# Optimization experiments

Hardware: AMD Instinct MI355X
Metric: run time of the kernel (lower is better)

The kernel has to match this reference:

```python
import jax, jax.numpy as jnp
import numpy as np

EPS_CIOU = 1e-7   # keras backend epsilon used inside compute_ciou
EPS = 1e-9        # label-encoder epsilon
ALPHA = 0.5
BETA = 6.0
NUM_CLASSES = 80
TOPK = 10


def compute_ciou(b1, b2):
    """Complete IoU between xyxy boxes b1 (gt) and b2 (pred), broadcastable (...,4)."""
    x1a, y1a, x2a, y2a = b1[..., 0], b1[..., 1], b1[..., 2], b1[..., 3]
    x1b, y1b, x2b, y2b = b2[..., 0], b2[..., 1], b2[..., 2], b2[..., 3]
    w1 = x2a - x1a
    h1 = y2a - y1a + EPS_CIOU
    w2 = x2b - x1b
    h2 = y2b - y1b + EPS_CIOU
    iw = jnp.clip(jnp.minimum(x2a, x2b) - jnp.maximum(x1a, x1b), 0.0, None)
    ih = jnp.clip(jnp.minimum(y2a, y2b) - jnp.maximum(y1a, y1b), 0.0, None)
    inter = iw * ih
    union = w1 * h1 + w2 * h2 - inter
    iou = inter / (union + EPS_CIOU)
    cw = jnp.maximum(x2a, x2b) - jnp.minimum(x1a, x1b)
    ch = jnp.maximum(y2a, y2b) - jnp.minimum(y1a, y1b)
    c2 = cw * cw + ch * ch + EPS_CIOU
    rho2 = ((x1b + x2b - x1a - x2a) ** 2 + (y1b + y2b - y1a - y2a) ** 2) / 4.0
    v = (4.0 / np.pi ** 2) * (jnp.arctan(w2 / h2) - jnp.arctan(w1 / h1)) ** 2
    a = v / (v - iou + (1.0 + EPS_CIOU))
    return iou - (rho2 / c2 + v * a)


def _forward(pd_scores, pd_bboxes, anc_points, gt_labels, gt_bboxes, mask_gt):
    B, A, C = pd_scores.shape
    M = gt_bboxes.shape[1]
    f32 = pd_scores.dtype
    mask_gt_b = mask_gt.astype(bool)                      # (B, M, 1)

    # --- candidate anchors whose center falls inside each gt box ---
    lt = gt_bboxes[:, :, None, :2]                        # (B, M, 1, 2)
    rb = gt_bboxes[:, :, None, 2:]
    anc = anc_points[None, None, :, :]                    # (1, 1, A, 2)
    deltas = jnp.concatenate([anc - lt, rb - anc], -1)    # (B, M, A, 4)
    mask_in_gts = deltas.min(-1) > EPS                    # (B, M, A)
    valid = mask_in_gts & mask_gt_b                       # (B, M, A)

    # --- alignment metric: score^alpha * ciou^beta ---
    ind = gt_labels.astype(jnp.int32)                     # (B, M)
    scores_g = jnp.take_along_axis(pd_scores, jnp.maximum(ind, 0)[:, None, :], axis=-1)  # (B, A, M)
    scores_g = jnp.where(ind[:, None, :] >= 0, scores_g, 0.0)
    scores_g = jnp.transpose(scores_g, (0, 2, 1))         # (B, M, A)
    bbox_scores = jnp.where(valid, scores_g, 0.0)
    iou = compute_ciou(gt_bboxes[:, :, None, :], pd_bboxes[:, None, :, :])  # (B, M, A)
    iou = jnp.maximum(iou, 0.0)
    overlaps = jnp.where(valid, iou, 0.0)
    align_metric = bbox_scores ** ALPHA * overlaps ** BETA

    # --- top-k anchor candidates per gt box ---
    _, topk_idxs = jax.lax.top_k(align_metric, TOPK)      # (B, M, K)
    topk_mask = jnp.broadcast_to(mask_gt_b, (B, M, TOPK))
    topk_idxs = jnp.where(topk_mask, topk_idxs, 0)
    bi = jnp.arange(B)[:, None, None]
    mi = jnp.arange(M)[None, :, None]
    counts = jnp.zeros((B, M, A), f32).at[bi, mi, topk_idxs].add(1.0)
    mask_topk = jnp.where(counts > 1, 0.0, counts)        # duplicates (masked gts) -> 0
    mask_pos = mask_topk * mask_in_gts.astype(f32) * mask_gt.astype(f32)  # (B, M, A)

    # --- break ties: anchor matched to >1 gt keeps highest-IoU gt ---
    fg_mask = mask_pos.sum(axis=1)                        # (B, A)
    mask_multi = jnp.broadcast_to(fg_mask[:, None, :] > 1, (B, M, A))
    is_max = jax.nn.one_hot(jnp.argmax(overlaps, axis=1), M, dtype=f32)  # (B, A, M)
    is_max = jnp.transpose(is_max, (0, 2, 1))             # (B, M, A)
    mask_pos = jnp.where(mask_multi, is_max, mask_pos)
    fg_mask = mask_pos.sum(axis=1)
    target_gt_idx = jnp.argmax(mask_pos, axis=1)          # (B, A)

    # --- gather targets ---
    flat_idx = target_gt_idx + jnp.arange(B, dtype=target_gt_idx.dtype)[:, None] * M
    target_bboxes = gt_bboxes.reshape(-1, 4)[flat_idx]    # (B, A, 4)
    target_labels = jnp.maximum(gt_labels.reshape(-1)[flat_idx], 0.0)
    target_scores = jax.nn.one_hot(target_labels.astype(jnp.int32), C, dtype=f32)  # (B, A, C)
    target_scores = jnp.where((fg_mask > 0)[..., None], target_scores, 0.0)

    # --- normalize class targets by alignment ---
    align_metric = align_metric * mask_pos
    pos_align = align_metric.max(axis=-1, keepdims=True)              # (B, M, 1)
    pos_overlaps = (overlaps * mask_pos).max(axis=-1, keepdims=True)  # (B, M, 1)
    norm = (align_metric * pos_overlaps / (pos_align + EPS)).max(axis=-2)[..., None]  # (B, A, 1)
    target_scores = target_scores * norm

    return (jax.lax.stop_gradient(target_bboxes),
            jax.lax.stop_gradient(target_scores),
            jax.lax.stop_gradient(fg_mask > 0))


def setup_inputs() -> dict:
    key = jax.random.key(0)
    k = jax.random.split(key, 6)
    B, A, C, M = 32, 8400, 80, 64
    IMG = 640.0
    pd_scores = jax.random.uniform(k[0], (B, A, C), jnp.float32)
    pb = jax.random.uniform(k[1], (B, A, 4), jnp.float32) * IMG
    pd_bboxes = jnp.concatenate([jnp.minimum(pb[..., :2], pb[..., 2:]),
                                 jnp.maximum(pb[..., :2], pb[..., 2:])], -1)
    anc_points = jax.random.uniform(k[2], (A, 2), jnp.float32) * IMG
    ctr = jax.random.uniform(k[3], (B, M, 2), jnp.float32) * IMG
    wh = jax.random.uniform(k[4], (B, M, 2), jnp.float32) * 200.0 + 20.0
    gt_bboxes = jnp.concatenate([ctr - wh / 2, ctr + wh / 2], -1)
    gt_labels = jax.random.randint(k[5], (B, M), 0, C).astype(jnp.float32)
    mask_gt = jnp.ones((B, M, 1), jnp.bool_)
    return {"pd_scores": pd_scores, "pd_bboxes": pd_bboxes, "anc_points": anc_points,
            "gt_labels": gt_labels, "gt_bboxes": gt_bboxes, "mask_gt": mask_gt}


def reference(pd_scores, pd_bboxes, anc_points, gt_labels, gt_bboxes, mask_gt):
    return _forward(pd_scores, pd_bboxes, anc_points, gt_labels, gt_bboxes, mask_gt)
```

## Files before the change

kernel.cpp:

```cpp
#include <hip/hip_runtime.h>
#include <cstdint>
#include <cstddef>

#define EPSC 1e-7f
#define EPS9 1e-9f
#define K4PI2 0.40528473456935108577f
#define NTOPK 10
#define GX 16
#define GY 16
#define NCELL (GX * GY)
#define POOLCAP 2048

__device__ __forceinline__ bool mask_at(const unsigned char* mb, int i, int wide) {
    if (wide) return reinterpret_cast<const unsigned int*>(mb)[i] != 0u;
    return mb[i] != 0;
}

__device__ __forceinline__ unsigned long long shfl_xor_u64(unsigned long long v, int off) {
    int lo = __shfl_xor((int)(unsigned)(v & 0xFFFFFFFFull), off);
    int hi = __shfl_xor((int)(unsigned)(v >> 32), off);
    return ((unsigned long long)(unsigned)hi << 32) | (unsigned)lo;
}

__device__ __forceinline__ unsigned lane_rank(unsigned long long ball) {
    return __builtin_amdgcn_mbcnt_hi((unsigned)(ball >> 32),
           __builtin_amdgcn_mbcnt_lo((unsigned)(ball & 0xFFFFFFFFull), 0u));
}

__device__ __forceinline__ float ciou_clip(float x1a, float y1a, float x2a, float y2a,
                                           float w1h1, float atan1,
                                           float4 pb, float at2) {
    float w2 = pb.z - pb.x, h2 = pb.w - pb.y + EPSC;
    float iw = fmaxf(fminf(x2a, pb.z) - fmaxf(x1a, pb.x), 0.f);
    float ih = fmaxf(fminf(y2a, pb.w) - fmaxf(y1a, pb.y), 0.f);
    float inter = iw * ih;
    float uni = w1h1 + w2 * h2 - inter;
    float iou = inter / (uni + EPSC);
    float cw = fmaxf(x2a, pb.z) - fminf(x1a, pb.x);
    float ch = fmaxf(y2a, pb.w) - fminf(y1a, pb.y);
    float c2 = cw * cw + ch * ch + EPSC;
    float dx = pb.x + pb.z - x1a - x2a;
    float dy = pb.y + pb.w - y1a - y2a;
    float rho2 = (dx * dx + dy * dy) * 0.25f;
    float dat = at2 - atan1;
    float vv = K4PI2 * dat * dat;
    float aa = vv / (vv - iou + (1.f + EPSC));
    return fmaxf(iou - (rho2 / c2 + vv * aa), 0.f);
}

__global__ __launch_bounds__(1024) void k_prep(
    const unsigned char* __restrict__ mask, int nmask, int* __restrict__ mode,
    const float* __restrict__ anc, int A,
    int* __restrict__ cell_start, int* __restrict__ binned, float* __restrict__ gp)
{
    __shared__ int h[NCELL];
    __shared__ int cs[NCELL + 1];
    __shared__ int cur[NCELL];
    __shared__ float rmnx[16], rmny[16], rmxx[16], rmxy[16];
    __shared__ float s_gp[4];
    __shared__ int bad;

    int tid = threadIdx.x;
    int lane = tid & 63, wid = tid >> 6;
    const float2* an2 = reinterpret_cast<const float2*>(anc);

    if (tid == 0) bad = 0;
    if (tid < NCELL) h[tid] = 0;
    __syncthreads();

    const unsigned int* mw = reinterpret_cast<const unsigned int*>(mask);
    int nw = nmask >> 2;
    for (int i = tid; i < nw; i += 1024) {
        unsigned int v = mw[i];
        if (v != 0u && v != 1u && v != 0x3f800000u) atomicOr(&bad, 1);
    }

    float mnx = 3e38f, mny = 3e38f, mxx = -3e38f, mxy = -3e38f;
    for (int i = tid; i < A; i += 1024) {
        float2 p = an2[i];
        mnx = fminf(mnx, p.x); mny = fminf(mny, p.y);
        mxx = fmaxf(mxx, p.x); mxy = fmaxf(mxy, p.y);
    }
#pragma unroll
    for (int off = 32; off; off >>= 1) {
        mnx = fminf(mnx, __shfl_xor(mnx, off));
        mny = fminf(mny, __shfl_xor(mny, off));
        mxx = fmaxf(mxx, __shfl_xor(mxx, off));
        mxy = fmaxf(mxy, __shfl_xor(mxy, off));
    }
    if (lane == 0) { rmnx[wid] = mnx; rmny[wid] = mny; rmxx[wid] = mxx; rmxy[wid] = mxy; }
    __syncthreads();
    if (tid == 0) {
        mode[0] = bad ? 0 : 1;
        float a = 3e38f, b2 = 3e38f, c = -3e38f, d = -3e38f;
        for (int i = 0; i < 16; ++i) {
            a = fminf(a, rmnx[i]); b2 = fminf(b2, rmny[i]);
            c = fmaxf(c, rmxx[i]); d = fmaxf(d, rmxy[i]);
        }
        float rx = fmaxf(c - a, 1e-6f), ry = fmaxf(d - b2, 1e-6f);
        s_gp[0] = a; s_gp[1] = b2;
        s_gp[2] = (float)GX / rx; s_gp[3] = (float)GY / ry;
        gp[0] = s_gp[0]; gp[1] = s_gp[1]; gp[2] = s_gp[2]; gp[3] = s_gp[3];
    }
    __syncthreads();
    float ox = s_gp[0], oy = s_gp[1], ivx = s_gp[2], ivy = s_gp[3];

    for (int i = tid; i < A; i += 1024) {
        float2 p = an2[i];
        int cx = min(GX - 1, max(0, (int)floorf((p.x - ox) * ivx)));
        int cy = min(GY - 1, max(0, (int)floorf((p.y - oy) * ivy)));
        atomicAdd(&h[cy * GX + cx], 1);
    }
    __syncthreads();
    if (wid == 0) {
        int base = 0;
        for (int ch = 0; ch < NCELL / 64; ++ch) {
            int v = h[ch * 64 + lane];
            int inc = v;
            for (int off = 1; off < 64; off <<= 1) {
                int u = __shfl_up(inc, off);
                if (lane >= off) inc += u;
            }
            cs[ch * 64 + lane] = base + inc - v;
            base += __shfl(inc, 63);
        }
        if (lane == 0) cs[NCELL] = base;
    }
    __syncthreads();
    if (tid <= NCELL) cell_start[tid] = cs[tid];
    if (tid < NCELL) cur[tid] = cs[tid];
    __syncthreads();
    for (int i = tid; i < A; i += 1024) {
        float2 p = an2[i];
        int cx = min(GX - 1, max(0, (int)floorf((p.x - ox) * ivx)));
        int cy = min(GY - 1, max(0, (int)floorf((p.y - oy) * ivy)));
        int slot = atomicAdd(&cur[cy * GX + cx], 1);
        binned[slot] = i;
    }
}

#define INTEST(ap) ((ap.x - x1a > EPS9) & (ap.y - y1a > EPS9) & \
                    (x2a - ap.x > EPS9) & (y2a - ap.y > EPS9))

__global__ __launch_bounds__(256) void k_sel(
    const float* __restrict__ pd_scores, const float* __restrict__ pd_bboxes,
    const float* __restrict__ anc, const float* __restrict__ gt_labels,
    const float* __restrict__ gt_bboxes, const unsigned char* __restrict__ mask_gt,
    const int* __restrict__ mode, const int* __restrict__ cell_start,
    const int* __restrict__ binned, const float* __restrict__ gp,
    int* __restrict__ count, int* __restrict__ win_idx, float* __restrict__ win_al,
    int* __restrict__ win_fl, int* __restrict__ ovf,
    int A, int C, int M, int B)
{
    __shared__ unsigned long long pool[POOLCAP];
    __shared__ int sP[GY + 1];
    __shared__ int sB[GY];
    __shared__ int s_n, s_ovf;

    int bid = blockIdx.x;
    int b = bid % B, m = bid / B;
    int row = b * M + m;
    if (!mask_at(mask_gt, row, mode[0])) return;
    int tid = threadIdx.x;
    int lane = tid & 63, wid = tid >> 6;

    float4 g = reinterpret_cast<const float4*>(gt_bboxes)[row];
    float x1a = g.x, y1a = g.y, x2a = g.z, y2a = g.w;
    float w1 = x2a - x1a, h1 = y2a - y1a + EPSC;
    float w1h1 = w1 * h1;
    float atan1 = atanf(w1 / h1);
    int lbl = (int)gt_labels[row];

    float ox = gp[0], oy = gp[1], ivx = gp[2], ivy = gp[3];
    int cx0 = min(GX - 1, max(0, (int)floorf((x1a - ox) * ivx)));
    int cx1 = min(GX - 1, max(0, (int)floorf((x2a - ox) * ivx)));
    int cy0 = min(GY - 1, max(0, (int)floorf((y1a - oy) * ivy)));
    int cy1 = min(GY - 1, max(0, (int)floorf((y2a - oy) * ivy)));
    int ns = cy1 - cy0 + 1;

    if (tid == 0) {
        s_n = 0; s_ovf = 0;
        int P = 0;
        for (int s2 = 0; s2 < ns; ++s2) {
            int cbase = (cy0 + s2) * GX;
            int S = cell_start[cbase + cx0];
            int E = cell_start[cbase + cx1 + 1];
            sP[s2] = P; sB[s2] = S - P; P += E - S;
        }
        sP[ns] = P;
    }
    __syncthreads();
    int L = sP[ns];

    const float2* an2 = reinterpret_cast<const float2*>(anc);
    const float4* pb4 = reinterpret_cast<const float4*>(pd_bboxes + (size_t)b * A * 4);
    const float*  ps  = pd_scores + (size_t)b * A * C;

    int sptr = 0;
    for (int f0 = tid; f0 < L; f0 += 1024) {
        int f1 = f0 + 256, f2 = f0 + 512, f3 = f0 + 768;
        bool o1 = f1 < L, o2 = f2 < L, o3 = f3 < L;
        while (f0 >= sP[sptr + 1]) ++sptr;
        int sl0 = sB[sptr] + f0;
        int sp = sptr;
        if (o1) { while (f1 >= sP[sp + 1]) ++sp; }
        int sl1 = sB[sp] + f1;
        if (o2) { while (f2 >= sP[sp + 1]) ++sp; }
        int sl2 = sB[sp] + f2;
        if (o3) { while (f3 >= sP[sp + 1]) ++sp; }
        int sl3 = sB[sp] + f3;

        int a0 = binned[sl0];
        int a1 = o1 ? binned[sl1] : 0;
        int a2 = o2 ? binned[sl2] : 0;
        int a3 = o3 ? binned[sl3] : 0;
        float2 ap0 = an2[a0], ap1 = an2[a1], ap2 = an2[a2], ap3 = an2[a3];
        bool in0 = INTEST(ap0);
        bool in1 = o1 & INTEST(ap1);
        bool in2 = o2 & INTEST(ap2);
        bool in3 = o3 & INTEST(ap3);

        float4 pb0, pb1, pb2, pb3;
        float sc0 = 0.f, sc1 = 0.f, sc2 = 0.f, sc3 = 0.f;
        if (in0) { pb0 = pb4[a0]; if (lbl >= 0) sc0 = ps[(size_t)a0 * C + lbl]; }
        if (in1) { pb1 = pb4[a1]; if (lbl >= 0) sc1 = ps[(size_t)a1 * C + lbl]; }
        if (in2) { pb2 = pb4[a2]; if (lbl >= 0) sc2 = ps[(size_t)a2 * C + lbl]; }
        if (in3) { pb3 = pb4[a3]; if (lbl >= 0) sc3 = ps[(size_t)a3 * C + lbl]; }

#define PROC(ink, ak, pbk, sck) { \
        unsigned long long key = 0; \
        if (ink) { \
            float w2 = pbk.z - pbk.x, h2 = pbk.w - pbk.y + EPSC; \
            float at2 = atanf(w2 / h2); \
            float ovl = ciou_clip(x1a, y1a, x2a, y2a, w1h1, atan1, pbk, at2); \
            float o2v = ovl * ovl; \
            float val = sqrtf(sck) * (o2v * o2v * o2v); \
            key = ((unsigned long long)__float_as_uint(val) << 32) | (unsigned)(~(unsigned)ak); \
        } \
        unsigned long long ball = __ballot(ink); \
        if (ball) { \
            int bs = 0; \
            if (lane == 0) bs = atomicAdd(&s_n, __popcll(ball)); \
            bs = __shfl(bs, 0); \
            if (ink) { \
                int pos = bs + (int)lane_rank(ball); \
                if (pos < POOLCAP) pool[pos] = key; else s_ovf = 1; \
            } \
        } }
        PROC(in0, a0, pb0, sc0)
        PROC(in1, a1, pb1, sc1)
        PROC(in2, a2, pb2, sc2)
        PROC(in3, a3, pb3, sc3)
#undef PROC
    }
    __syncthreads();
    if (s_ovf || s_n > POOLCAP) {
        if (tid == 0) ovf[row] = 1;
        return;
    }
    if (wid != 0) return;

    int n = s_n;
    unsigned long long tv[NTOPK];
#pragma unroll
    for (int j = 0; j < NTOPK; ++j) tv[j] = 0;
    int pcnt = 0;
    for (int i = lane; i < n; i += 64) {
        unsigned long long kk = pool[i];
        pcnt += (kk >> 32) ? 1 : 0;
        if (kk > tv[NTOPK - 1]) {
            tv[NTOPK - 1] = kk;
#pragma unroll
            for (int j = NTOPK - 1; j > 0; --j)
                if (tv[j] > tv[j - 1]) { unsigned long long t = tv[j]; tv[j] = tv[j - 1]; tv[j - 1] = t; }
        }
    }
#pragma unroll
    for (int off = 32; off; off >>= 1) pcnt += __shfl_xor(pcnt, off);
    int p = pcnt;
    int rp = p < NTOPK ? p : NTOPK;
    size_t bA = (size_t)b * A;
    int base_o = row * NTOPK;

    for (int k = 0; k < rp; ++k) {
        unsigned long long head = tv[0];
        unsigned long long best = head;
#pragma unroll
        for (int off = 32; off; off >>= 1) {
            unsigned long long o = shfl_xor_u64(best, off);
            if (o > best) best = o;
        }
        if (head == best && head != 0ull) {
            int a = (int)(~(unsigned)(best & 0xFFFFFFFFull));
            int o = base_o + k;
            win_idx[o] = a;
            win_al[o]  = __uint_as_float((unsigned)(best >> 32));
            win_fl[o]  = 1;
            atomicAdd(&count[bA + a], 1);
#pragma unroll
            for (int j = 0; j < NTOPK - 1; ++j) tv[j] = tv[j + 1];
            tv[NTOPK - 1] = 0;
        }
    }

    if (rp < NTOPK) {
        int iters = (A + 63 - lane) / 64;
        int zp = 0;
        for (int k = rp; k < NTOPK; ++k) {
            unsigned zprop = 0xFFFFFFFFu;
            while (zp < iters) {
                int a = lane + zp * 64;
                float2 ap = an2[a];
                bool in = INTEST(ap);
                if (!in) { zprop = (unsigned)a; break; }
                ++zp;
            }
            unsigned cprop = 0xFFFFFFFFu;
#pragma unroll
            for (int j = 0; j < NTOPK; ++j) {
                unsigned long long kk = tv[j];
                if (kk != 0ull && kk < (1ull << 32)) {
                    unsigned idx2 = ~(unsigned)kk;
                    if (idx2 < cprop) cprop = idx2;
                }
            }
            unsigned prop = zprop < cprop ? zprop : cprop;
            unsigned bm_ = prop;
#pragma unroll
            for (int off = 32; off; off >>= 1) {
                unsigned o = (unsigned)__shfl_xor((int)bm_, off);
                if (o < bm_) bm_ = o;
            }
            if (bm_ != 0xFFFFFFFFu) {
                if (cprop == bm_ && cprop < zprop) {
                    int o = base_o + k;
                    win_idx[o] = (int)bm_; win_al[o] = 0.f; win_fl[o] = 1;
                    atomicAdd(&count[bA + bm_], 1);
                    unsigned long long wkk = (unsigned long long)(unsigned)(~bm_);
#pragma unroll
                    for (int j = 0; j < NTOPK; ++j) if (tv[j] == wkk) tv[j] = 0;
                } else if (zprop == bm_ && zprop < cprop) {
                    ++zp;
                }
            }
        }
    }
}

__global__ __launch_bounds__(64) void k_sel_fb(
    const float* __restrict__ pd_scores, const float* __restrict__ pd_bboxes,
    const float* __restrict__ anc, const float* __restrict__ gt_labels,
    const float* __restrict__ gt_bboxes, const unsigned char* __restrict__ mask_gt,
    const int* __restrict__ mode, const int* __restrict__ cell_start,
    const int* __restrict__ binned, const float* __restrict__ gp,
    const int* __restrict__ ovf,
    int* __restrict__ count, int* __restrict__ win_idx, float* __restrict__ win_al,
    int* __restrict__ win_fl,
    int A, int C, int M)
{
    int row = blockIdx.x;
    if (!ovf[row]) return;
    if (!mask_at(mask_gt, row, mode[0])) return;
    int b = row / M;
    int lane = threadIdx.x;

    float4 g = reinterpret_cast<const float4*>(gt_bboxes)[row];
    float x1a = g.x, y1a = g.y, x2a = g.z, y2a = g.w;
    float w1 = x2a - x1a, h1 = y2a - y1a + EPSC;
    float w1h1 = w1 * h1;
    float atan1 = atanf(w1 / h1);
    int lbl = (int)gt_labels[row];

    float ox = gp[0], oy = gp[1], ivx = gp[2], ivy = gp[3];
    int cx0 = min(GX - 1, max(0, (int)floorf((x1a - ox) * ivx)));
    int cx1 = min(GX - 1, max(0, (int)floorf((x2a - ox) * ivx)));
    int cy0 = min(GY - 1, max(0, (int)floorf((y1a - oy) * ivy)));
    int cy1 = min(GY - 1, max(0, (int)floorf((y2a - oy) * ivy)));

    const float2* an2 = reinterpret_cast<const float2*>(anc);
    const float4* pb4 = reinterpret_cast<const float4*>(pd_bboxes + (size_t)b * A * 4);
    const float*  ps  = pd_scores + (size_t)b * A * C;

    unsigned long long tv[NTOPK];
#pragma unroll
    for (int j = 0; j < NTOPK; ++j) tv[j] = 0;
    int pcnt = 0;

    for (int cy = cy0; cy <= cy1; ++cy) {
        int c0 = cy * GX + cx0;
        int s = cell_start[c0], e = cell_start[cy * GX + cx1 + 1];
        for (int i = s + lane; i < e; i += 64) {
            int a = binned[i];
            float2 ap = an2[a];
            bool in = INTEST(ap);
            if (in) {
                float4 pb = pb4[a];
                float w2 = pb.z - pb.x, h2 = pb.w - pb.y + EPSC;
                float at2 = atanf(w2 / h2);
                float ovl = ciou_clip(x1a, y1a, x2a, y2a, w1h1, atan1, pb, at2);
                float sc = (lbl >= 0) ? ps[(size_t)a * C + lbl] : 0.f;
                float o2 = ovl * ovl;
                float val = sqrtf(sc) * (o2 * o2 * o2);
                pcnt += (val > 0.f) ? 1 : 0;
                unsigned long long kk =
                    ((unsigned long long)__float_as_uint(val) << 32) | (unsigned)(~(unsigned)a);
                if (kk > tv[NTOPK - 1]) {
                    tv[NTOPK - 1] = kk;
#pragma unroll
                    for (int j = NTOPK - 1; j > 0; --j)
                        if (tv[j] > tv[j - 1]) {
                            unsigned long long t = tv[j]; tv[j] = tv[j - 1]; tv[j - 1] = t;
                        }
                }
            }
        }
    }

#pragma unroll
    for (int off = 32; off; off >>= 1) pcnt += __shfl_xor(pcnt, off);
    int p = pcnt;
    int rp = p < NTOPK ? p : NTOPK;
    size_t bA = (size_t)b * A;
    int base_o = row * NTOPK;

    for (int k = 0; k < rp; ++k) {
        unsigned long long head = tv[0];
        unsigned long long best = head;
#pragma unroll
        for (int off = 32; off; off >>= 1) {
            unsigned long long o = shfl_xor_u64(best, off);
            if (o > best) best = o;
        }
        if (head == best && head != 0ull) {
            int a = (int)(~(unsigned)(best & 0xFFFFFFFFull));
            int o = base_o + k;
            win_idx[o] = a;
            win_al[o]  = __uint_as_float((unsigned)(best >> 32));
            win_fl[o]  = 1;
            atomicAdd(&count[bA + a], 1);
#pragma unroll
            for (int j = 0; j < NTOPK - 1; ++j) tv[j] = tv[j + 1];
            tv[NTOPK - 1] = 0;
        }
    }

    if (rp < NTOPK) {
        int iters = (A + 63 - lane) / 64;
        int zp = 0;
        for (int k = rp; k < NTOPK; ++k) {
            unsigned zprop = 0xFFFFFFFFu;
            while (zp < iters) {
                int a = lane + zp * 64;
                float2 ap = an2[a];
                bool in = INTEST(ap);
                if (!in) { zprop = (unsigned)a; break; }
                ++zp;
            }
            unsigned cprop = 0xFFFFFFFFu;
#pragma unroll
            for (int j = 0; j < NTOPK; ++j) {
                unsigned long long kk = tv[j];
                if (kk != 0ull && kk < (1ull << 32)) {
                    unsigned idx2 = ~(unsigned)kk;
                    if (idx2 < cprop) cprop = idx2;
                }
            }
            unsigned prop = zprop < cprop ? zprop : cprop;
            unsigned bm_ = prop;
#pragma unroll
            for (int off = 32; off; off >>= 1) {
                unsigned o = (unsigned)__shfl_xor((int)bm_, off);
                if (o < bm_) bm_ = o;
            }
            if (bm_ != 0xFFFFFFFFu) {
                if (cprop == bm_ && cprop < zprop) {
                    int o = base_o + k;
                    win_idx[o] = (int)bm_; win_al[o] = 0.f; win_fl[o] = 1;
                    atomicAdd(&count[bA + bm_], 1);
                    unsigned long long wkk = (unsigned long long)(unsigned)(~bm_);
#pragma unroll
                    for (int j = 0; j < NTOPK; ++j) if (tv[j] == wkk) tv[j] = 0;
                } else if (zprop == bm_ && zprop < cprop) {
                    ++zp;
                }
            }
        }
    }
}

__global__ void k_resolve(
    const float* __restrict__ pd_scores, const float* __restrict__ pd_bboxes,
    const float* __restrict__ anc, const float* __restrict__ gt_labels,
    const float* __restrict__ gt_bboxes, const unsigned char* __restrict__ mask_gt,
    const int* __restrict__ mode,
    const int* __restrict__ count, const int* __restrict__ win_idx,
    const float* __restrict__ win_al, const int* __restrict__ win_fl,
    int* __restrict__ claim_m, float* __restrict__ claim_al,
    float* __restrict__ pos_al, float* __restrict__ pos_ov,
    int A, int C, int M, int total)
{
    int t = blockIdx.x * 256 + threadIdx.x;
    if (t >= total) return;
    int bm = t / NTOPK;
    int b = bm / M, m = bm % M;
    if (!win_fl[t]) return;
    int a = win_idx[t];
    size_t ba = (size_t)b * A + a;
    int cnt = count[ba];
    float al, ov; int mm_out;
    if (cnt == 1) {
        mm_out = m; al = win_al[t];
        float4 gg = reinterpret_cast<const float4*>(gt_bboxes)[b * M + m];
        float w1 = gg.z - gg.x, h1 = gg.w - gg.y + EPSC;
        float4 pb = reinterpret_cast<const float4*>(pd_bboxes)[ba];
        float w2 = pb.z - pb.x, h2p = pb.w - pb.y + EPSC;
        ov = ciou_clip(gg.x, gg.y, gg.z, gg.w, w1 * h1, atanf(w1 / h1), pb, atanf(w2 / h2p));
    } else {
        int wide = mode[0];
        float4 pb = reinterpret_cast<const float4*>(pd_bboxes)[ba];
        float2 ap = reinterpret_cast<const float2*>(anc)[a];
        float w2 = pb.z - pb.x, h2p = pb.w - pb.y + EPSC;
        float at2 = atanf(w2 / h2p);
        float best_ov = -1.f; int best_m = 0, best_valid = 0;
        for (int mm = 0; mm < M; ++mm) {
            float4 gg = reinterpret_cast<const float4*>(gt_bboxes)[b * M + mm];
            bool in = (ap.x - gg.x > EPS9) && (ap.y - gg.y > EPS9) &&
                      (gg.z - ap.x > EPS9) && (gg.w - ap.y > EPS9);
            bool valid = in && mask_at(mask_gt, b * M + mm, wide);
            float ovv = 0.f;
            if (valid) {
                float w1 = gg.z - gg.x, h1 = gg.w - gg.y + EPSC;
                ovv = ciou_clip(gg.x, gg.y, gg.z, gg.w, w1 * h1, atanf(w1 / h1), pb, at2);
            }
            if (ovv > best_ov) { best_ov = ovv; best_m = mm; best_valid = valid ? 1 : 0; }
        }
        int lb = (int)gt_labels[b * M + best_m];
        float sc = (best_valid && lb >= 0) ? pd_scores[ba * C + lb] : 0.f;
        float o2 = best_ov * best_ov;
        mm_out = best_m; al = sqrtf(sc) * (o2 * o2 * o2); ov = best_ov;
    }
    claim_m[ba]  = mm_out;
    claim_al[ba] = al;
    atomicMax((unsigned int*)&pos_al[b * M + mm_out], __float_as_uint(al));
    atomicMax((unsigned int*)&pos_ov[b * M + mm_out], __float_as_uint(ov));
}

__global__ __launch_bounds__(256) void k_final(
    const int* __restrict__ count, const int* __restrict__ claim_m,
    const float* __restrict__ claim_al,
    const float* __restrict__ pos_al, const float* __restrict__ pos_ov,
    const float* __restrict__ gt_labels, const float* __restrict__ gt_bboxes,
    float* __restrict__ out_bb, float* __restrict__ out_ts, float* __restrict__ out_fg,
    int A, int M, int C4, int BA)
{
    __shared__ float s_nv[256];
    __shared__ int   s_lb[256];
    int base_ba = blockIdx.x * 256;
    int tid = threadIdx.x;
    int ba = base_ba + tid;
    if (ba < BA) {
        int b = ba / A;
        int cnt = count[ba];
        int m = claim_m[ba];
        float4 g = reinterpret_cast<const float4*>(gt_bboxes)[b * M + m];
        reinterpret_cast<float4*>(out_bb)[ba] = g;
        float nv = 0.f; int lb = -1;
        if (cnt > 0) {
            lb = max((int)gt_labels[b * M + m], 0);
            nv = claim_al[ba] * pos_ov[b * M + m] / (pos_al[b * M + m] + EPS9);
        }
        out_fg[ba] = (cnt > 0) ? 1.f : 0.f;
        s_nv[tid] = nv; s_lb[tid] = lb;
    } else { s_nv[tid] = 0.f; s_lb[tid] = -1; }
    __syncthreads();
    float4* ts4 = reinterpret_cast<float4*>(out_ts);
    size_t fbase = (size_t)base_ba * C4;
    for (int j = 0; j < C4; ++j) {
        int fl = j * 256 + tid;
        int la = fl / C4;
        int ch = fl - la * C4;
        int ba2 = base_ba + la;
        if (ba2 < BA) {
            float nv = s_nv[la];
            int lb = s_lb[la];
            int c0 = ch * 4;
            float4 o;
            o.x = (c0     == lb) ? nv : 0.f;
            o.y = (c0 + 1 == lb) ? nv : 0.f;
            o.z = (c0 + 2 == lb) ? nv : 0.f;
            o.w = (c0 + 3 == lb) ? nv : 0.f;
            ts4[fbase + fl] = o;
        }
    }
}

extern "C" void kernel_launch(void* const* d_in, const int* in_sizes, int n_in,
                              void* d_out, int out_size, void* d_ws, size_t ws_size,
                              hipStream_t stream) {
    const float* pd_scores = (const float*)d_in[0];
    const float* pd_bboxes = (const float*)d_in[1];
    const float* anc       = (const float*)d_in[2];
    const float* gt_labels = (const float*)d_in[3];
    const float* gt_bboxes = (const float*)d_in[4];
    const unsigned char* mask_gt = (const unsigned char*)d_in[5];

    int A  = in_sizes[2] / 2;
    int BA = in_sizes[1] / 4;
    int B  = BA / A;
    int C  = in_sizes[0] / BA;
    int M  = in_sizes[3] / B;
    int BM = B * M;

    char* w = (char*)d_ws;
    auto alloc = [&](size_t bytes) { char* p = w; w += ((bytes + 255) / 256) * 256; return p; };
    int*   mode       = (int*)  alloc(256);
    char*  zero_beg   = w;
    int*   count      = (int*)  alloc((size_t)BA * 4);
    int*   claim_m    = (int*)  alloc((size_t)BA * 4);
    float* pos_al     = (float*)alloc((size_t)BM * 4);
    float* pos_ov     = (float*)alloc((size_t)BM * 4);
    int*   win_fl     = (int*)  alloc((size_t)BM * NTOPK * 4);
    int*   ovf        = (int*)  alloc((size_t)BM * 4);
    char*  zero_end   = w;
    float* claim_al   = (float*)alloc((size_t)BA * 4);
    int*   win_idx    = (int*)  alloc((size_t)BM * NTOPK * 4);
    float* win_al     = (float*)alloc((size_t)BM * NTOPK * 4);
    int*   cell_start = (int*)  alloc((size_t)(NCELL + 1) * 4);
    int*   binned     = (int*)  alloc((size_t)A * 4);
    float* gp         = (float*)alloc(256);

    float* out_bb = (float*)d_out;
    float* out_ts = out_bb + (size_t)BA * 4;
    float* out_fg = out_ts + (size_t)BA * C;

    hipMemsetAsync(zero_beg, 0, (size_t)(zero_end - zero_beg), stream);

    k_prep<<<1, 1024, 0, stream>>>(mask_gt, BM, mode, anc, A, cell_start, binned, gp);
    k_sel<<<BM, 256, 0, stream>>>(pd_scores, pd_bboxes, anc, gt_labels, gt_bboxes, mask_gt,
                                  mode, cell_start, binned, gp,
                                  count, win_idx, win_al, win_fl, ovf, A, C, M, B);
    k_sel_fb<<<BM, 64, 0, stream>>>(pd_scores, pd_bboxes, anc, gt_labels, gt_bboxes, mask_gt,
                                    mode, cell_start, binned, gp, ovf,
                                    count, win_idx, win_al, win_fl, A, C, M);
    int nclaims = BM * NTOPK;
    k_resolve<<<(nclaims + 255) / 256, 256, 0, stream>>>(
        pd_scores, pd_bboxes, anc, gt_labels, gt_bboxes, mask_gt, mode,
        count, win_idx, win_al, win_fl, claim_m, claim_al, pos_al, pos_ov, A, C, M, nclaims);
    int C4 = C / 4;
    int gBA = (BA + 255) / 256;
    k_final<<<gBA, 256, 0, stream>>>(count, claim_m, claim_al, pos_al, pos_ov,
                                     gt_labels, gt_bboxes, out_bb, out_ts, out_fg, A, M, C4, BA);
}
```

Baseline: 97.08 us.

## Fold fallback into selection kernel, zero outputs separately, sparse target-score writes

The separate overflow fallback kernel is removed; overflowing rows now run the warp-level scan inline inside k_sel, which eliminates one launch and the ovf buffer. The workspace memset becomes a custom zeroing kernel, and a second zeroing kernel clears the whole dense target-score output. The final kernel then writes only the single nonzero class per positive anchor instead of composing every float4 of the dense output. claim_m is moved out of the zeroed range and is read only when the count is positive. Box loads in k_sel are made unconditional so they can be issued early, at the cost of extra loads for anchors that fail the in-box test.

```diff
diff --git a/kernel.cpp b/kernel.cpp
--- a/kernel.cpp
+++ b/kernel.cpp
@@ -48,6 +48,11 @@
     return fmaxf(iou - (rho2 / c2 + vv * aa), 0.f);
 }
 
+__global__ void k_zero(float4* __restrict__ p, int n4) {
+    int i = blockIdx.x * 256 + threadIdx.x;
+    if (i < n4) p[i] = make_float4(0.f, 0.f, 0.f, 0.f);
+}
+
 __global__ __launch_bounds__(1024) void k_prep(
     const unsigned char* __restrict__ mask, int nmask, int* __restrict__ mode,
     const float* __restrict__ anc, int A,
@@ -142,6 +147,111 @@
 #define INTEST(ap) ((ap.x - x1a > EPS9) & (ap.y - y1a > EPS9) & \
                     (x2a - ap.x > EPS9) & (y2a - ap.y > EPS9))
 
+__device__ void fb_scan(
+    int lane, int A, int C, float x1a, float y1a, float x2a, float y2a,
+    float w1h1, float atan1, int lbl,
+    int cx0, int cx1, int cy0, int cy1,
+    const float2* an2, const float4* pb4, const float* ps,
+    const int* cell_start, const int* binned,
+    int* count, int* win_idx, float* win_al, int* win_fl,
+    size_t bA, int base_o)
+{
+    unsigned long long tv[NTOPK];
+#pragma unroll
+    for (int j = 0; j < NTOPK; ++j) tv[j] = 0;
+    int pcnt = 0;
+    for (int cy = cy0; cy <= cy1; ++cy) {
+        int s = cell_start[cy * GX + cx0], e = cell_start[cy * GX + cx1 + 1];
+        for (int i = s + lane; i < e; i += 64) {
+            int a = binned[i];
+            float2 ap = an2[a];
+            bool in = INTEST(ap);
+            if (in) {
+                float4 pb = pb4[a];
+                float w2 = pb.z - pb.x, h2 = pb.w - pb.y + EPSC;
+                float at2 = atanf(w2 / h2);
+                float ovl = ciou_clip(x1a, y1a, x2a, y2a, w1h1, atan1, pb, at2);
+                float sc = (lbl >= 0) ? ps[(size_t)a * C + lbl] : 0.f;
+                float o2 = ovl * ovl;
+                float val = sqrtf(sc) * (o2 * o2 * o2);
+                pcnt += (val > 0.f) ? 1 : 0;
+                unsigned long long kk =
+                    ((unsigned long long)__float_as_uint(val) << 32) | (unsigned)(~(unsigned)a);
+                if (kk > tv[NTOPK - 1]) {
+                    tv[NTOPK - 1] = kk;
+#pragma unroll
+                    for (int j = NTOPK - 1; j > 0; --j)
+                        if (tv[j] > tv[j - 1]) {
+                            unsigned long long t = tv[j]; tv[j] = tv[j - 1]; tv[j - 1] = t;
+                        }
+                }
+            }
+        }
+    }
+#pragma unroll
+    for (int off = 32; off; off >>= 1) pcnt += __shfl_xor(pcnt, off);
+    int rp = pcnt < NTOPK ? pcnt : NTOPK;
+    for (int k = 0; k < rp; ++k) {
+        unsigned long long head = tv[0];
+        unsigned long long best = head;
+#pragma unroll
+        for (int off = 32; off; off >>= 1) {
+            unsigned long long o = shfl_xor_u64(best, off);
+            if (o > best) best = o;
+        }
+        if (head == best && head != 0ull) {
+            int a = (int)(~(unsigned)(best & 0xFFFFFFFFull));
+            int o = base_o + k;
+            win_idx[o] = a; win_al[o] = __uint_as_float((unsigned)(best >> 32)); win_fl[o] = 1;
+            atomicAdd(&count[bA + a], 1);
+#pragma unroll
+            for (int j = 0; j < NTOPK - 1; ++j) tv[j] = tv[j + 1];
+            tv[NTOPK - 1] = 0;
+        }
+    }
+    if (rp < NTOPK) {
+        int iters = (A + 63 - lane) / 64;
+        int zp = 0;
+        for (int k = rp; k < NTOPK; ++k) {
+            unsigned zprop = 0xFFFFFFFFu;
+            while (zp < iters) {
+                int a = lane + zp * 64;
+                float2 ap = an2[a];
+                if (!INTEST(ap)) { zprop = (unsigned)a; break; }
+                ++zp;
+            }
+            unsigned cprop = 0xFFFFFFFFu;
+#pragma unroll
+            for (int j = 0; j < NTOPK; ++j) {
+                unsigned long long kk = tv[j];
+                if (kk != 0ull && kk < (1ull << 32)) {
+                    unsigned idx2 = ~(unsigned)kk;
+                    if (idx2 < cprop) cprop = idx2;
+                }
+            }
+            unsigned prop = zprop < cprop ? zprop : cprop;
+            unsigned bm_ = prop;
+#pragma unroll
+            for (int off = 32; off; off >>= 1) {
+                unsigned o = (unsigned)__shfl_xor((int)bm_, off);
+                if (o < bm_) bm_ = o;
+            }
+            if (bm_ != 0xFFFFFFFFu) {
+                if (cprop == bm_ && cprop < zprop) {
+                    int o = base_o + k;
+                    win_idx[o] = (int)bm_; win_al[o] = 0.f; win_fl[o] = 1;
+                    atomicAdd(&count[bA + bm_], 1);
+                    unsigned long long wkk = (unsigned long long)(unsigned)(~bm_);
+#pragma unroll
+                    for (int j = 0; j < NTOPK; ++j) if (tv[j] == wkk) tv[j] = 0;
+                } else if (zprop == bm_ && zprop < cprop) {
+                    ++zp;
+                }
+            }
+        }
+    }
+}
+
 __global__ __launch_bounds__(256) void k_sel(
     const float* __restrict__ pd_scores, const float* __restrict__ pd_bboxes,
     const float* __restrict__ anc, const float* __restrict__ gt_labels,
@@ -149,7 +259,7 @@
     const int* __restrict__ mode, const int* __restrict__ cell_start,
     const int* __restrict__ binned, const float* __restrict__ gp,
     int* __restrict__ count, int* __restrict__ win_idx, float* __restrict__ win_al,
-    int* __restrict__ win_fl, int* __restrict__ ovf,
+    int* __restrict__ win_fl,
     int A, int C, int M, int B)
 {
     __shared__ unsigned long long pool[POOLCAP];
@@ -157,8 +267,8 @@
     __shared__ int sB[GY];
     __shared__ int s_n, s_ovf;
 
-    int bid = blockIdx.x;
-    int b = bid % B, m = bid / B;
+    int rid = blockIdx.x;
+    int b = rid % B, m = rid / B;
     int row = b * M + m;
     if (!mask_at(mask_gt, row, mode[0])) return;
     int tid = threadIdx.x;
@@ -195,6 +305,8 @@
     const float2* an2 = reinterpret_cast<const float2*>(anc);
     const float4* pb4 = reinterpret_cast<const float4*>(pd_bboxes + (size_t)b * A * 4);
     const float*  ps  = pd_scores + (size_t)b * A * C;
+    size_t bA = (size_t)b * A;
+    int base_o = row * NTOPK;
 
     int sptr = 0;
     for (int f0 = tid; f0 < L; f0 += 1024) {
@@ -215,17 +327,17 @@
         int a2 = o2 ? binned[sl2] : 0;
         int a3 = o3 ? binned[sl3] : 0;
         float2 ap0 = an2[a0], ap1 = an2[a1], ap2 = an2[a2], ap3 = an2[a3];
+        float4 pb0 = pb4[a0], pb1 = pb4[a1], pb2 = pb4[a2], pb3 = pb4[a3];
         bool in0 = INTEST(ap0);
         bool in1 = o1 & INTEST(ap1);
         bool in2 = o2 & INTEST(ap2);
         bool in3 = o3 & INTEST(ap3);
 
-        float4 pb0, pb1, pb2, pb3;
         float sc0 = 0.f, sc1 = 0.f, sc2 = 0.f, sc3 = 0.f;
-        if (in0) { pb0 = pb4[a0]; if (lbl >= 0) sc0 = ps[(size_t)a0 * C + lbl]; }
-        if (in1) { pb1 = pb4[a1]; if (lbl >= 0) sc1 = ps[(size_t)a1 * C + lbl]; }
-        if (in2) { pb2 = pb4[a2]; if (lbl >= 0) sc2 = ps[(size_t)a2 * C + lbl]; }
-        if (in3) { pb3 = pb4[a3]; if (lbl >= 0) sc3 = ps[(size_t)a3 * C + lbl]; }
+        if (in0 && lbl >= 0) sc0 = ps[(size_t)a0 * C + lbl];
+        if (in1 && lbl >= 0) sc1 = ps[(size_t)a1 * C + lbl];
+        if (in2 && lbl >= 0) sc2 = ps[(size_t)a2 * C + lbl];
+        if (in3 && lbl >= 0) sc3 = ps[(size_t)a3 * C + lbl];
 
 #define PROC(ink, ak, pbk, sck) { \
         unsigned long long key = 0; \
@@ -255,7 +367,10 @@
     }
     __syncthreads();
     if (s_ovf || s_n > POOLCAP) {
-        if (tid == 0) ovf[row] = 1;
+        if (wid == 0)
+            fb_scan(lane, A, C, x1a, y1a, x2a, y2a, w1h1, atan1, lbl,
+                    cx0, cx1, cy0, cy1, an2, pb4, ps, cell_start, binned,
+                    count, win_idx, win_al, win_fl, bA, base_o);
         return;
     }
     if (wid != 0) return;
@@ -279,8 +394,6 @@
     for (int off = 32; off; off >>= 1) pcnt += __shfl_xor(pcnt, off);
     int p = pcnt;
     int rp = p < NTOPK ? p : NTOPK;
-    size_t bA = (size_t)b * A;
-    int base_o = row * NTOPK;
 
     for (int k = 0; k < rp; ++k) {
         unsigned long long head = tv[0];
@@ -311,149 +424,7 @@
             while (zp < iters) {
                 int a = lane + zp * 64;
                 float2 ap = an2[a];
-                bool in = INTEST(ap);
-                if (!in) { zprop = (unsigned)a; break; }
-                ++zp;
-            }
-            unsigned cprop = 0xFFFFFFFFu;
-#pragma unroll
-            for (int j = 0; j < NTOPK; ++j) {
-                unsigned long long kk = tv[j];
-                if (kk != 0ull && kk < (1ull << 32)) {
-                    unsigned idx2 = ~(unsigned)kk;
-                    if (idx2 < cprop) cprop = idx2;
-                }
-            }
-            unsigned prop = zprop < cprop ? zprop : cprop;
-            unsigned bm_ = prop;
-#pragma unroll
-            for (int off = 32; off; off >>= 1) {
-                unsigned o = (unsigned)__shfl_xor((int)bm_, off);
-                if (o < bm_) bm_ = o;
-            }
-            if (bm_ != 0xFFFFFFFFu) {
-                if (cprop == bm_ && cprop < zprop) {
-                    int o = base_o + k;
-                    win_idx[o] = (int)bm_; win_al[o] = 0.f; win_fl[o] = 1;
-                    atomicAdd(&count[bA + bm_], 1);
-                    unsigned long long wkk = (unsigned long long)(unsigned)(~bm_);
-#pragma unroll
-                    for (int j = 0; j < NTOPK; ++j) if (tv[j] == wkk) tv[j] = 0;
-                } else if (zprop == bm_ && zprop < cprop) {
-                    ++zp;
-                }
-            }
-        }
-    }
-}
-
-__global__ __launch_bounds__(64) void k_sel_fb(
-    const float* __restrict__ pd_scores, const float* __restrict__ pd_bboxes,
-    const float* __restrict__ anc, const float* __restrict__ gt_labels,
-    const float* __restrict__ gt_bboxes, const unsigned char* __restrict__ mask_gt,
-    const int* __restrict__ mode, const int* __restrict__ cell_start,
-    const int* __restrict__ binned, const float* __restrict__ gp,
-    const int* __restrict__ ovf,
-    int* __restrict__ count, int* __restrict__ win_idx, float* __restrict__ win_al,
-    int* __restrict__ win_fl,
-    int A, int C, int M)
-{
-    int row = blockIdx.x;
-    if (!ovf[row]) return;
-    if (!mask_at(mask_gt, row, mode[0])) return;
-    int b = row / M;
-    int lane = threadIdx.x;
-
-    float4 g = reinterpret_cast<const float4*>(gt_bboxes)[row];
-    float x1a = g.x, y1a = g.y, x2a = g.z, y2a = g.w;
-    float w1 = x2a - x1a, h1 = y2a - y1a + EPSC;
-    float w1h1 = w1 * h1;
-    float atan1 = atanf(w1 / h1);
-    int lbl = (int)gt_labels[row];
-
-    float ox = gp[0], oy = gp[1], ivx = gp[2], ivy = gp[3];
-    int cx0 = min(GX - 1, max(0, (int)floorf((x1a - ox) * ivx)));
-    int cx1 = min(GX - 1, max(0, (int)floorf((x2a - ox) * ivx)));
-    int cy0 = min(GY - 1, max(0, (int)floorf((y1a - oy) * ivy)));
-    int cy1 = min(GY - 1, max(0, (int)floorf((y2a - oy) * ivy)));
-
-    const float2* an2 = reinterpret_cast<const float2*>(anc);
-    const float4* pb4 = reinterpret_cast<const float4*>(pd_bboxes + (size_t)b * A * 4);
-    const float*  ps  = pd_scores + (size_t)b * A * C;
-
-    unsigned long long tv[NTOPK];
-#pragma unroll
-    for (int j = 0; j < NTOPK; ++j) tv[j] = 0;
-    int pcnt = 0;
-
-    for (int cy = cy0; cy <= cy1; ++cy) {
-        int c0 = cy * GX + cx0;
-        int s = cell_start[c0], e = cell_start[cy * GX + cx1 + 1];
-        for (int i = s + lane; i < e; i += 64) {
-            int a = binned[i];
-            float2 ap = an2[a];
-            bool in = INTEST(ap);
-            if (in) {
-                float4 pb = pb4[a];
-                float w2 = pb.z - pb.x, h2 = pb.w - pb.y + EPSC;
-                float at2 = atanf(w2 / h2);
-                float ovl = ciou_clip(x1a, y1a, x2a, y2a, w1h1, atan1, pb, at2);
-                float sc = (lbl >= 0) ? ps[(size_t)a * C + lbl] : 0.f;
-                float o2 = ovl * ovl;
-                float val = sqrtf(sc) * (o2 * o2 * o2);
-                pcnt += (val > 0.f) ? 1 : 0;
-                unsigned long long kk =
-                    ((unsigned long long)__float_as_uint(val) << 32) | (unsigned)(~(unsigned)a);
-                if (kk > tv[NTOPK - 1]) {
-                    tv[NTOPK - 1] = kk;
-#pragma unroll
-                    for (int j = NTOPK - 1; j > 0; --j)
-                        if (tv[j] > tv[j - 1]) {
-                            unsigned long long t = tv[j]; tv[j] = tv[j - 1]; tv[j - 1] = t;
-                        }
-                }
-            }
-        }
-    }
-
-#pragma unroll
-    for (int off = 32; off; off >>= 1) pcnt += __shfl_xor(pcnt, off);
-    int p = pcnt;
-    int rp = p < NTOPK ? p : NTOPK;
-    size_t bA = (size_t)b * A;
-    int base_o = row * NTOPK;
-
-    for (int k = 0; k < rp; ++k) {
-        unsigned long long head = tv[0];
-        unsigned long long best = head;
-#pragma unroll
-        for (int off = 32; off; off >>= 1) {
-            unsigned long long o = shfl_xor_u64(best, off);
-            if (o > best) best = o;
-        }
-        if (head == best && head != 0ull) {
-            int a = (int)(~(unsigned)(best & 0xFFFFFFFFull));
-            int o = base_o + k;
-            win_idx[o] = a;
-            win_al[o]  = __uint_as_float((unsigned)(best >> 32));
-            win_fl[o]  = 1;
-            atomicAdd(&count[bA + a], 1);
-#pragma unroll
-            for (int j = 0; j < NTOPK - 1; ++j) tv[j] = tv[j + 1];
-            tv[NTOPK - 1] = 0;
-        }
-    }
-
-    if (rp < NTOPK) {
-        int iters = (A + 63 - lane) / 64;
-        int zp = 0;
-        for (int k = rp; k < NTOPK; ++k) {
-            unsigned zprop = 0xFFFFFFFFu;
-            while (zp < iters) {
-                int a = lane + zp * 64;
-                float2 ap = an2[a];
-                bool in = INTEST(ap);
-                if (!in) { zprop = (unsigned)a; break; }
+                if (!INTEST(ap)) { zprop = (unsigned)a; break; }
                 ++zp;
             }
             unsigned cprop = 0xFFFFFFFFu;
@@ -545,52 +516,26 @@
     atomicMax((unsigned int*)&pos_ov[b * M + mm_out], __float_as_uint(ov));
 }
 
-__global__ __launch_bounds__(256) void k_final(
+__global__ __launch_bounds__(256) void k_final_small(
     const int* __restrict__ count, const int* __restrict__ claim_m,
     const float* __restrict__ claim_al,
     const float* __restrict__ pos_al, const float* __restrict__ pos_ov,
     const float* __restrict__ gt_labels, const float* __restrict__ gt_bboxes,
     float* __restrict__ out_bb, float* __restrict__ out_ts, float* __restrict__ out_fg,
-    int A, int M, int C4, int BA)
+    int A, int M, int C, int BA)
 {
-    __shared__ float s_nv[256];
-    __shared__ int   s_lb[256];
-    int base_ba = blockIdx.x * 256;
-    int tid = threadIdx.x;
-    int ba = base_ba + tid;
-    if (ba < BA) {
-        int b = ba / A;
-        int cnt = count[ba];
-        int m = claim_m[ba];
-        float4 g = reinterpret_cast<const float4*>(gt_bboxes)[b * M + m];
-        reinterpret_cast<float4*>(out_bb)[ba] = g;
-        float nv = 0.f; int lb = -1;
-        if (cnt > 0) {
-            lb = max((int)gt_labels[b * M + m], 0);
-            nv = claim_al[ba] * pos_ov[b * M + m] / (pos_al[b * M + m] + EPS9);
-        }
-        out_fg[ba] = (cnt > 0) ? 1.f : 0.f;
-        s_nv[tid] = nv; s_lb[tid] = lb;
-    } else { s_nv[tid] = 0.f; s_lb[tid] = -1; }
-    __syncthreads();
-    float4* ts4 = reinterpret_cast<float4*>(out_ts);
-    size_t fbase = (size_t)base_ba * C4;
-    for (int j = 0; j < C4; ++j) {
-        int fl = j * 256 + tid;
-        int la = fl / C4;
-        int ch = fl - la * C4;
-        int ba2 = base_ba + la;
-        if (ba2 < BA) {
-            float nv = s_nv[la];
-            int lb = s_lb[la];
-            int c0 = ch * 4;
-            float4 o;
-            o.x = (c0     == lb) ? nv : 0.f;
-            o.y = (c0 + 1 == lb) ? nv : 0.f;
-            o.z = (c0 + 2 == lb) ? nv : 0.f;
-            o.w = (c0 + 3 == lb) ? nv : 0.f;
-            ts4[fbase + fl] = o;
-        }
+    int ba = blockIdx.x * 256 + threadIdx.x;
+    if (ba >= BA) return;
+    int b = ba / A;
+    int cnt = count[ba];
+    int m = (cnt > 0) ? claim_m[ba] : 0;
+    float4 g = reinterpret_cast<const float4*>(gt_bboxes)[b * M + m];
+    reinterpret_cast<float4*>(out_bb)[ba] = g;
+    out_fg[ba] = (cnt > 0) ? 1.f : 0.f;
+    if (cnt > 0) {
+        int lb = max((int)gt_labels[b * M + m], 0);
+        float nv = claim_al[ba] * pos_ov[b * M + m] / (pos_al[b * M + m] + EPS9);
+        out_ts[(size_t)ba * C + lb] = nv;
     }
 }
 
@@ -616,12 +561,11 @@
     int*   mode       = (int*)  alloc(256);
     char*  zero_beg   = w;
     int*   count      = (int*)  alloc((size_t)BA * 4);
-    int*   claim_m    = (int*)  alloc((size_t)BA * 4);
     float* pos_al     = (float*)alloc((size_t)BM * 4);
     float* pos_ov     = (float*)alloc((size_t)BM * 4);
     int*   win_fl     = (int*)  alloc((size_t)BM * NTOPK * 4);
-    int*   ovf        = (int*)  alloc((size_t)BM * 4);
     char*  zero_end   = w;
+    int*   claim_m    = (int*)  alloc((size_t)BA * 4);
     float* claim_al   = (float*)alloc((size_t)BA * 4);
     int*   win_idx    = (int*)  alloc((size_t)BM * NTOPK * 4);
     float* win_al     = (float*)alloc((size_t)BM * NTOPK * 4);
@@ -633,21 +577,21 @@
     float* out_ts = out_bb + (size_t)BA * 4;
     float* out_fg = out_ts + (size_t)BA * C;
 
-    hipMemsetAsync(zero_beg, 0, (size_t)(zero_end - zero_beg), stream);
+    int n4ws = (int)((size_t)(zero_end - zero_beg) / 16);
+    k_zero<<<(n4ws + 255) / 256, 256, 0, stream>>>((float4*)zero_beg, n4ws);
+    int n4ts = (int)((size_t)BA * C / 4);
+    k_zero<<<(n4ts + 255) / 256, 256, 0, stream>>>((float4*)out_ts, n4ts);
 
     k_prep<<<1, 1024, 0, stream>>>(mask_gt, BM, mode, anc, A, cell_start, binned, gp);
     k_sel<<<BM, 256, 0, stream>>>(pd_scores, pd_bboxes, anc, gt_labels, gt_bboxes, mask_gt,
                                   mode, cell_start, binned, gp,
-                                  count, win_idx, win_al, win_fl, ovf, A, C, M, B);
-    k_sel_fb<<<BM, 64, 0, stream>>>(pd_scores, pd_bboxes, anc, gt_labels, gt_bboxes, mask_gt,
-                                    mode, cell_start, binned, gp, ovf,
-                                    count, win_idx, win_al, win_fl, A, C, M);
+                                  count, win_idx, win_al, win_fl, A, C, M, B);
     int nclaims = BM * NTOPK;
     k_resolve<<<(nclaims + 255) / 256, 256, 0, stream>>>(
         pd_scores, pd_bboxes, anc, gt_labels, gt_bboxes, mask_gt, mode,
         count, win_idx, win_al, win_fl, claim_m, claim_al, pos_al, pos_ov, A, C, M, nclaims);
-    int C4 = C / 4;
     int gBA = (BA + 255) / 256;
-    k_final<<<gBA, 256, 0, stream>>>(count, claim_m, claim_al, pos_al, pos_ov,
-                                     gt_labels, gt_bboxes, out_bb, out_ts, out_fg, A, M, C4, BA);
-}
+    k_final_small<<<gBA, 256, 0, stream>>>(count, claim_m, claim_al, pos_al, pos_ov,
+                                           gt_labels, gt_bboxes, out_bb, out_ts, out_fg,
+                                           A, M, C, BA);
+}
```

New measurement: 96.98 us. No clear change (-0.1%).
